# Kernel optimization log

Measured on AMD Instinct MI355X. Metric: run time of the kernel, lower is better.

## Reference

```python
import jax, jax.numpy as jnp
import numpy as np

T = 16777216  # series length (2**24)


def setup_inputs() -> dict:
    key = jax.random.key(0)
    k1, k2 = jax.random.split(key)
    timeseries = jax.random.normal(k1, (T,), dtype=jnp.float32)
    # learned smoothing parameter alpha in (0, 1), per min_max_norm(0, 1) constraint
    alpha = jax.random.uniform(k2, (1,), dtype=jnp.float32)
    return {"timeseries": timeseries, "alpha": alpha}


def reference(timeseries, alpha):
    """Simple exponential smoothing (component form).

    level_0 = y_0; level_t = (1-alpha)*level_{t-1} + alpha*y_t for t >= 1.
    prediction_t (the forecast emitted at step t) is the level BEFORE the
    update, so the output is levels[0 : T-1], length T-1 (matches the
    original loop that emits one forecast per timestep in timeseries[1:]).

    Expressed as a first-order linear recurrence s_t = a_t * s_{t-1} + b_t
    and solved with an associative (parallel) scan.
    """
    a0 = alpha[0]
    n = timeseries.shape[0]
    dt = timeseries.dtype
    # a_0 = 0, b_0 = y_0 pins level_0 = y_0 regardless of the dummy carry.
    a = jnp.concatenate([jnp.zeros((1,), dt),
                         jnp.full((n - 1,), 1.0, dt) * (1.0 - a0)])
    b = jnp.concatenate([timeseries[:1], a0 * timeseries[1:]])

    def combine(e1, e2):
        a1, b1 = e1
        a2, b2 = e2
        return (a1 * a2, a2 * b1 + b2)

    _, levels = jax.lax.associative_scan(combine, (a, b))  # levels[t] = level_t
    return levels[:-1]
```

## Files before the change

### kernel.cpp

```cpp
#include <hip/hip_runtime.h>
#include <stdint.h>


#define BLOCK 256
#define SEG   64
#define VPT   (SEG / 4)
#define CHUNK (BLOCK * SEG)
#define ROWS  65

__device__ __forceinline__ void block_scan_affine(float* sa, float* sb, int t) {
#pragma unroll
    for (int off = 1; off < BLOCK; off <<= 1) {
        float pa = 1.0f, pb = 0.0f;
        if (t >= off) { pa = sa[t - off]; pb = sb[t - off]; }
        __syncthreads();
        if (t >= off) {
            float ca = sa[t], cb = sb[t];
            sa[t] = pa * ca;
            sb[t] = fmaf(ca, pb, cb);
        }
        __syncthreads();
    }
}

__global__ __launch_bounds__(BLOCK) void k_block_agg(
    const float* __restrict__ y, const float* __restrict__ alpha_p,
    float* __restrict__ aggA, float* __restrict__ aggB, long n)
{
    const int t = threadIdx.x;
    const long base = (long)blockIdx.x * CHUNK + (long)t * SEG;
    const float alpha = alpha_p[0];
    const float oma = 1.0f - alpha;

    float a = 1.0f, s = 0.0f;
    if (base + SEG <= n) {
        const float4* p = (const float4*)(y + base);
#pragma unroll
        for (int v = 0; v < VPT; ++v) {
            float4 q = p[v];
            s = fmaf(oma, s, alpha * q.x);
            s = fmaf(oma, s, alpha * q.y);
            s = fmaf(oma, s, alpha * q.z);
            s = fmaf(oma, s, alpha * q.w);
        }
        a = __powf(oma, (float)SEG);
    } else {
        for (int k = 0; k < SEG; ++k) {
            long idx = base + k;
            if (idx < n) { s = fmaf(oma, s, alpha * y[idx]); a *= oma; }
        }
    }

    __shared__ float sa[BLOCK], sb[BLOCK];
    sa[t] = a; sb[t] = s;
    __syncthreads();
    block_scan_affine(sa, sb, t);
    if (t == BLOCK - 1) {
        aggA[blockIdx.x] = sa[t];
        aggB[blockIdx.x] = sb[t];
    }
}

__global__ __launch_bounds__(BLOCK, 4) void k_emit_fused(
    const float* __restrict__ y, const float* __restrict__ alpha_p,
    const float* __restrict__ aggA, const float* __restrict__ aggB,
    float* __restrict__ out, long n, int G)
{
    __shared__ float sa[BLOCK], sb[BLOCK];
    __shared__ float stage[2 * 64 * ROWS];
    __shared__ float s_carry;

    const int t = threadIdx.x;
    const int tile = blockIdx.x;
    const float alpha = alpha_p[0];
    const float oma   = 1.0f - alpha;
    const long tbase = (long)tile * CHUNK;
    const long base  = tbase + (long)t * SEG;
    const bool fullTile = (tbase + CHUNK <= n);
    const float y0 = y[0];

    float4 arr[VPT];
    float a_seg, b_seg;
    if (fullTile) {
        const float4* p = (const float4*)(y + base);
#pragma unroll
        for (int v = 0; v < VPT; ++v) arr[v] = p[v];
        float s = 0.0f;
#pragma unroll
        for (int v = 0; v < VPT; ++v) {
            s = fmaf(oma, s, alpha * arr[v].x);
            s = fmaf(oma, s, alpha * arr[v].y);
            s = fmaf(oma, s, alpha * arr[v].z);
            s = fmaf(oma, s, alpha * arr[v].w);
        }
        b_seg = s;
        a_seg = __powf(oma, (float)SEG);
    } else {
        float a = 1.0f, s = 0.0f;
        for (int k = 0; k < SEG; ++k) {
            long idx = base + k;
            if (idx < n) { s = fmaf(oma, s, alpha * y[idx]); a *= oma; }
        }
        a_seg = a; b_seg = s;
    }

    sa[t] = a_seg; sb[t] = b_seg;
    __syncthreads();
    block_scan_affine(sa, sb, t);

    float ea_th = 1.0f, eb_th = 0.0f;
    if (t > 0) { ea_th = sa[t - 1]; eb_th = sb[t - 1]; }

    const int items = (G + BLOCK - 1) / BLOCK;
    {
        float ta = 1.0f, tb = 0.0f;
        for (int j = 0; j < items; ++j) {
            int g = t * items + j;
            if (g < G) {
                float ca = aggA[g], cb = aggB[g];
                tb = fmaf(ca, tb, cb);
                ta *= ca;
            }
        }
        __syncthreads();
        sa[t] = ta; sb[t] = tb;
        __syncthreads();
        block_scan_affine(sa, sb, t);

        const int q = tile / items;
        if (t == q) {
            float ea = (q > 0) ? sa[q - 1] : 1.0f;
            float eb = (q > 0) ? sb[q - 1] : 0.0f;
            const int r = tile - q * items;
            for (int j = 0; j < r; ++j) {
                int g = q * items + j;
                float ca = aggA[g], cb = aggB[g];
                eb = fmaf(ca, eb, cb);
                ea *= ca;
            }
            s_carry = fmaf(ea, y0, eb);
        }
        __syncthreads();
    }

    float lvl = fmaf(ea_th, s_carry, eb_th);

    if (fullTile) {
#pragma unroll
        for (int v = 0; v < VPT; ++v) {
            float4 q4 = arr[v], r;
            lvl = fmaf(oma, lvl, alpha * q4.x); r.x = lvl;
            lvl = fmaf(oma, lvl, alpha * q4.y); r.y = lvl;
            lvl = fmaf(oma, lvl, alpha * q4.z); r.z = lvl;
            lvl = fmaf(oma, lvl, alpha * q4.w); r.w = lvl;
            arr[v] = r;
        }
        const int  wv = t >> 6;
        const int  ln = t & 63;
        const bool lastGuard = (tbase + CHUNK > n - 1);
#pragma unroll
        for (int p = 0; p < 2; ++p) {
            __syncthreads();
            if ((wv >> 1) == p) {
                int g = ((wv & 1) << 6) | ln;
                float* row = &stage[g * ROWS];
#pragma unroll
                for (int v = 0; v < VPT; ++v) {
                    row[4 * v + 0] = arr[v].x;
                    row[4 * v + 1] = arr[v].y;
                    row[4 * v + 2] = arr[v].z;
                    row[4 * v + 3] = arr[v].w;
                }
            }
            __syncthreads();
            const long rbase = tbase + (long)p * 8192;
#pragma unroll
            for (int k = 0; k < 8; ++k) {
                int jj = t + (k << 8);
                int g  = jj >> 4;
                int e  = (jj << 2) & 63;
                const float* row = &stage[g * ROWS + e];
                float4 r;
                r.x = row[0]; r.y = row[1]; r.z = row[2]; r.w = row[3];
                long gi = rbase + 4 * (long)jj;
                if (!lastGuard) {
                    *(float4*)(out + gi) = r;
                } else {
                    if (gi + 4 <= n - 1) {
                        *(float4*)(out + gi) = r;
                    } else {
                        if (gi + 0 < n - 1) out[gi + 0] = r.x;
                        if (gi + 1 < n - 1) out[gi + 1] = r.y;
                        if (gi + 2 < n - 1) out[gi + 2] = r.z;
                        if (gi + 3 < n - 1) out[gi + 3] = r.w;
                    }
                }
            }
        }
    } else {
        for (int k = 0; k < SEG; ++k) {
            long idx = base + k;
            if (idx < n) {
                lvl = fmaf(oma, lvl, alpha * y[idx]);
                if (idx < n - 1) out[idx] = lvl;
            }
        }
    }
}

extern "C" void kernel_launch(void* const* d_in, const int* in_sizes, int n_in,
                              void* d_out, int out_size, void* d_ws, size_t ws_size,
                              hipStream_t stream) {
    const float* y     = (const float*)d_in[0];
    const float* alpha = (const float*)d_in[1];
    float* out = (float*)d_out;
    const long n = (long)in_sizes[0];
    const int  G = (int)((n + CHUNK - 1) / CHUNK);

    float* aggA = (float*)d_ws;
    float* aggB = aggA + G;

    k_block_agg<<<G, BLOCK, 0, stream>>>(y, alpha, aggA, aggB, n);
    k_emit_fused<<<G, BLOCK, 0, stream>>>(y, alpha, aggA, aggB, out, n, G);
}
```

Before: 129.2 us.

## Fuse aggregate and emit passes into one kernel with atomic grid barrier

Replaces the two-kernel scan with a single kernel. Each block publishes its chunk aggregate, then all blocks wait on a hierarchical atomic counter barrier before combining the aggregates into their carry. This removes the second full read of the input series and one kernel launch. The staging buffer is halved, so the LDS write-out takes four rounds. It depends on all blocks being co-resident, and it adds a memset and spin-wait latency.

```diff
diff --git a/kernel.cpp b/kernel.cpp
--- a/kernel.cpp
+++ b/kernel.cpp
@@ -23,51 +23,17 @@
     }
 }
 
-__global__ __launch_bounds__(BLOCK) void k_block_agg(
+__global__ __launch_bounds__(BLOCK, 4) void k_ses_onepass(
     const float* __restrict__ y, const float* __restrict__ alpha_p,
-    float* __restrict__ aggA, float* __restrict__ aggB, long n)
-{
-    const int t = threadIdx.x;
-    const long base = (long)blockIdx.x * CHUNK + (long)t * SEG;
-    const float alpha = alpha_p[0];
-    const float oma = 1.0f - alpha;
-
-    float a = 1.0f, s = 0.0f;
-    if (base + SEG <= n) {
-        const float4* p = (const float4*)(y + base);
-#pragma unroll
-        for (int v = 0; v < VPT; ++v) {
-            float4 q = p[v];
-            s = fmaf(oma, s, alpha * q.x);
-            s = fmaf(oma, s, alpha * q.y);
-            s = fmaf(oma, s, alpha * q.z);
-            s = fmaf(oma, s, alpha * q.w);
-        }
-        a = __powf(oma, (float)SEG);
-    } else {
-        for (int k = 0; k < SEG; ++k) {
-            long idx = base + k;
-            if (idx < n) { s = fmaf(oma, s, alpha * y[idx]); a *= oma; }
-        }
-    }
-
-    __shared__ float sa[BLOCK], sb[BLOCK];
-    sa[t] = a; sb[t] = s;
-    __syncthreads();
-    block_scan_affine(sa, sb, t);
-    if (t == BLOCK - 1) {
-        aggA[blockIdx.x] = sa[t];
-        aggB[blockIdx.x] = sb[t];
-    }
-}
-
-__global__ __launch_bounds__(BLOCK, 4) void k_emit_fused(
-    const float* __restrict__ y, const float* __restrict__ alpha_p,
-    const float* __restrict__ aggA, const float* __restrict__ aggB,
-    float* __restrict__ out, long n, int G)
+    float* __restrict__ out,
+    int* __restrict__ cnt,
+    int* __restrict__ root,
+    int* __restrict__ flag,
+    float2* __restrict__ agg,
+    long n, int G)
 {
     __shared__ float sa[BLOCK], sb[BLOCK];
-    __shared__ float stage[2 * 64 * ROWS];
+    __shared__ float stage[64 * ROWS];
     __shared__ float s_carry;
 
     const int t = threadIdx.x;
@@ -111,18 +77,43 @@
     float ea_th = 1.0f, eb_th = 0.0f;
     if (t > 0) { ea_th = sa[t - 1]; eb_th = sb[t - 1]; }
 
+    if (t == BLOCK - 1) {
+        float2 ab; ab.x = sa[t]; ab.y = sb[t];
+        agg[tile] = ab;
+        __threadfence();
+    }
+    __syncthreads();
+
+    if (t == 0) {
+        const int grp   = tile >> 5;
+        const int gbase = grp << 5;
+        const int gsz   = (G - gbase < 32) ? (G - gbase) : 32;
+        const int ngrp  = (G + 31) >> 5;
+        int old = __hip_atomic_fetch_add(&cnt[grp], 1, __ATOMIC_RELEASE, __HIP_MEMORY_SCOPE_AGENT);
+        if (old == gsz - 1) {
+            int old2 = __hip_atomic_fetch_add(root, 1, __ATOMIC_ACQ_REL, __HIP_MEMORY_SCOPE_AGENT);
+            if (old2 == ngrp - 1) {
+                __hip_atomic_store(flag, 1, __ATOMIC_RELEASE, __HIP_MEMORY_SCOPE_AGENT);
+            }
+        }
+        while (__hip_atomic_load(flag, __ATOMIC_ACQUIRE, __HIP_MEMORY_SCOPE_AGENT) == 0) {
+            __builtin_amdgcn_s_sleep(1);
+        }
+        __threadfence();
+    }
+    __syncthreads();
+
     const int items = (G + BLOCK - 1) / BLOCK;
     {
         float ta = 1.0f, tb = 0.0f;
         for (int j = 0; j < items; ++j) {
             int g = t * items + j;
             if (g < G) {
-                float ca = aggA[g], cb = aggB[g];
-                tb = fmaf(ca, tb, cb);
-                ta *= ca;
-            }
-        }
-        __syncthreads();
+                float2 ab = agg[g];
+                tb = fmaf(ab.x, tb, ab.y);
+                ta *= ab.x;
+            }
+        }
         sa[t] = ta; sb[t] = tb;
         __syncthreads();
         block_scan_affine(sa, sb, t);
@@ -133,10 +124,9 @@
             float eb = (q > 0) ? sb[q - 1] : 0.0f;
             const int r = tile - q * items;
             for (int j = 0; j < r; ++j) {
-                int g = q * items + j;
-                float ca = aggA[g], cb = aggB[g];
-                eb = fmaf(ca, eb, cb);
-                ea *= ca;
+                float2 ab = agg[q * items + j];
+                eb = fmaf(ab.x, eb, ab.y);
+                ea *= ab.x;
             }
             s_carry = fmaf(ea, y0, eb);
         }
@@ -159,11 +149,10 @@
         const int  ln = t & 63;
         const bool lastGuard = (tbase + CHUNK > n - 1);
 #pragma unroll
-        for (int p = 0; p < 2; ++p) {
+        for (int p = 0; p < 4; ++p) {
             __syncthreads();
-            if ((wv >> 1) == p) {
-                int g = ((wv & 1) << 6) | ln;
-                float* row = &stage[g * ROWS];
+            if (wv == p) {
+                float* row = &stage[ln * ROWS];
 #pragma unroll
                 for (int v = 0; v < VPT; ++v) {
                     row[4 * v + 0] = arr[v].x;
@@ -173,9 +162,9 @@
                 }
             }
             __syncthreads();
-            const long rbase = tbase + (long)p * 8192;
-#pragma unroll
-            for (int k = 0; k < 8; ++k) {
+            const long rbase = tbase + (long)p * 4096;
+#pragma unroll
+            for (int k = 0; k < 4; ++k) {
                 int jj = t + (k << 8);
                 int g  = jj >> 4;
                 int e  = (jj << 2) & 63;
@@ -217,9 +206,12 @@
     const long n = (long)in_sizes[0];
     const int  G = (int)((n + CHUNK - 1) / CHUNK);
 
-    float* aggA = (float*)d_ws;
-    float* aggB = aggA + G;
-
-    k_block_agg<<<G, BLOCK, 0, stream>>>(y, alpha, aggA, aggB, n);
-    k_emit_fused<<<G, BLOCK, 0, stream>>>(y, alpha, aggA, aggB, out, n, G);
+    char* ws = (char*)d_ws;
+    int*    cnt  = (int*)ws;
+    int*    root = (int*)(ws + 256);
+    int*    flg  = (int*)(ws + 384);
+    float2* agg  = (float2*)(ws + 512);
+
+    hipMemsetAsync(d_ws, 0, 512, stream);
+    k_ses_onepass<<<G, BLOCK, 0, stream>>>(y, alpha, out, cnt, root, flg, agg, n, G);
 }
```

Result: slower. 239.3 us (+85.3%).
